# Kernel tuning notes

Measured on AMD Instinct MI355X. Metric: run time of the kernel, lower is better.

## Reference

```python
import jax, jax.numpy as jnp
import numpy as np

D = 512
H = 8
DH = D // H
DFF = 2048
SLOTS = 1024
TOPK = 5
LN_EPS = 1e-5
NORM_EPS = 1e-12


def setup_inputs() -> dict:
    key = jax.random.key(0)
    ks = jax.random.split(key, 12)
    B, S = 8, 1024
    inp = {
        "src": jax.random.normal(ks[0], (B, S, D), dtype=jnp.float32),
        # MultiheadAttention params (torch layout: in_proj [3D, D], out_proj [D, D])
        "in_proj_w": jax.random.normal(ks[1], (3 * D, D), dtype=jnp.float32) * 0.02,
        "in_proj_b": jnp.zeros((3 * D,), dtype=jnp.float32),
        "out_proj_w": jax.random.normal(ks[2], (D, D), dtype=jnp.float32) * 0.02,
        "out_proj_b": jnp.zeros((D,), dtype=jnp.float32),
        # BPBookMemory params
        "memory": jax.random.normal(ks[3], (SLOTS, D), dtype=jnp.float32),
        "retrieval_scale": jnp.asarray(0.1, dtype=jnp.float32),
        # LayerNorms
        "ln1_g": jnp.ones((D,), dtype=jnp.float32),
        "ln1_b": jnp.zeros((D,), dtype=jnp.float32),
        "ln2_g": jnp.ones((D,), dtype=jnp.float32),
        "ln2_b": jnp.zeros((D,), dtype=jnp.float32),
        # FFN (torch Linear layout: [out, in])
        "w1": jax.random.normal(ks[4], (DFF, D), dtype=jnp.float32) * 0.02,
        "b1": jnp.zeros((DFF,), dtype=jnp.float32),
        "w2": jax.random.normal(ks[5], (D, DFF), dtype=jnp.float32) * 0.02,
        "b2": jnp.zeros((D,), dtype=jnp.float32),
    }
    return inp


def _layer_norm(x, g, b):
    mu = jnp.mean(x, axis=-1, keepdims=True)
    var = jnp.var(x, axis=-1, keepdims=True)
    return (x - mu) * jax.lax.rsqrt(var + LN_EPS) * g + b


def _l2_normalize(x):
    n = jnp.linalg.norm(x, axis=-1, keepdims=True)
    return x / jnp.maximum(n, NORM_EPS)


def _forward(src, in_proj_w, in_proj_b, out_proj_w, out_proj_b,
             memory, retrieval_scale, ln1_g, ln1_b, ln2_g, ln2_b,
             w1, b1, w2, b2):
    B, S, _ = src.shape
    # ---- pre-norm self-attention ----
    h = _layer_norm(src, ln1_g, ln1_b)
    qkv = h @ in_proj_w.T + in_proj_b            # [B,S,3D]
    q, k, v = jnp.split(qkv, 3, axis=-1)
    q = q.reshape(B, S, H, DH)
    k = k.reshape(B, S, H, DH)
    v = v.reshape(B, S, H, DH)
    scores = jnp.einsum("bqhd,bkhd->bhqk", q, k) / jnp.sqrt(jnp.float32(DH))
    attn = jax.nn.softmax(scores, axis=-1)
    ctx = jnp.einsum("bhqk,bkhd->bqhd", attn, v).reshape(B, S, D)
    attn_out = ctx @ out_proj_w.T + out_proj_b
    src = src + attn_out
    # ---- BP-Book memory: cosine sim -> topk -> softmax -> gather -> weighted sum ----
    xn = _l2_normalize(src)                      # [B,S,D]
    mn = _l2_normalize(memory)                   # [SLOTS,D]
    sim = xn @ mn.T                              # [B,S,SLOTS]
    topk_scores, topk_idx = jax.lax.top_k(sim, TOPK)
    w = jax.nn.softmax(topk_scores, axis=-1)     # [B,S,TOPK]
    retrieved = memory[topk_idx]                 # [B,S,TOPK,D]
    weighted = jnp.einsum("bskd,bsk->bsd", retrieved, w)
    src = src + retrieval_scale * weighted
    # ---- FFN ----
    h = _layer_norm(src, ln2_g, ln2_b)
    ffn = jax.nn.gelu(h @ w1.T + b1, approximate=False) @ w2.T + b2
    return src + ffn


def reference(src, in_proj_w, in_proj_b, out_proj_w, out_proj_b,
              memory, retrieval_scale, ln1_g, ln1_b, ln2_g, ln2_b,
              w1, b1, w2, b2):
    return _forward(src, in_proj_w, in_proj_b, out_proj_w, out_proj_b,
                    memory, retrieval_scale, ln1_g, ln1_b, ln2_g, ln2_b,
                    w1, b1, w2, b2)
```

## Files before the change

kernel.cpp:

```cpp
#include <hip/hip_runtime.h>
#include <math.h>

#define D_ 512
#define H_ 8
#define DFF_ 2048
#define SLOTS_ 1024
#define TOPK_ 5
#define NCAND_ 8
#define NTOK_ 8192
#define SEQ_ 1024
#define LN_EPS_ 1e-5f

typedef __attribute__((ext_vector_type(8))) short bf16x8;
typedef __attribute__((ext_vector_type(4))) float f32x4;
typedef __attribute__((ext_vector_type(4))) unsigned u32x4;

__device__ inline void split2(float x, unsigned short& hi, unsigned short& lo) {
    unsigned u = __builtin_bit_cast(unsigned, x);
    hi = (unsigned short)(u >> 16);
    float h = __builtin_bit_cast(float, u & 0xFFFF0000u);
    float rem = x - h;
    lo = (unsigned short)(__builtin_bit_cast(unsigned, rem) >> 16);
}

__device__ __forceinline__ void gld16(const void* g, void* l) {
    __builtin_amdgcn_global_load_lds(
        (const __attribute__((address_space(1))) void*)g,
        (__attribute__((address_space(3))) void*)l, 16, 0, 0);
}

__device__ __forceinline__ int SW7(int r) { return (r ^ (r >> 3)) & 7; }
__device__ __forceinline__ const bf16x8* frag(const unsigned short* p, int r, int c) {
    return (const bf16x8*)(p + r * 64 + ((c ^ SW7(r)) << 3));
}

__global__ __launch_bounds__(256) void splitall_kernel(
    const float* __restrict__ inw, const float* __restrict__ outw,
    const float* __restrict__ w1, const float* __restrict__ w2,
    unsigned short* __restrict__ inwh, unsigned short* __restrict__ inwl,
    unsigned short* __restrict__ outwh, unsigned short* __restrict__ outwl,
    unsigned short* __restrict__ w1h, unsigned short* __restrict__ w2h)
{
    const int i = (blockIdx.x * 256 + threadIdx.x) * 4;
    const float* x;
    unsigned short *hh, *ll;
    int base;
    if (i < 786432)       { x = inw;  hh = inwh;  ll = inwl;  base = 0; }
    else if (i < 1048576) { x = outw; hh = outwh; ll = outwl; base = 786432; }
    else if (i < 2097152) { x = w1;   hh = w1h;   ll = nullptr; base = 1048576; }
    else                  { x = w2;   hh = w2h;   ll = nullptr; base = 2097152; }
    const int j = i - base;
    const float4 v = *(const float4*)(x + j);
    const float vv[4] = {v.x, v.y, v.z, v.w};
    unsigned short h[4], l[4];
#pragma unroll
    for (int e = 0; e < 4; ++e) split2(vv[e], h[e], l[e]);
    hh[j + 0] = h[0]; hh[j + 1] = h[1]; hh[j + 2] = h[2]; hh[j + 3] = h[3];
    if (ll) { ll[j + 0] = l[0]; ll[j + 1] = l[1]; ll[j + 2] = l[2]; ll[j + 3] = l[3]; }
}

__global__ __launch_bounds__(256) void ln_kernel(
    const float* __restrict__ x, const float* __restrict__ g,
    const float* __restrict__ be, unsigned short* __restrict__ yh,
    unsigned short* __restrict__ yl)
{
    const int row = blockIdx.x;
    const int t = threadIdx.x;
    const float a = x[(size_t)row * D_ + t];
    const float b = x[(size_t)row * D_ + t + 256];
    float s = a + b;
    float ss = a * a + b * b;
#pragma unroll
    for (int off = 32; off; off >>= 1) {
        s += __shfl_xor(s, off);
        ss += __shfl_xor(ss, off);
    }
    __shared__ float rs[4], rss[4];
    if ((t & 63) == 0) { rs[t >> 6] = s; rss[t >> 6] = ss; }
    __syncthreads();
    s = rs[0] + rs[1] + rs[2] + rs[3];
    ss = rss[0] + rss[1] + rss[2] + rss[3];
    const float mu = s * (1.0f / D_);
    const float var = ss * (1.0f / D_) - mu * mu;
    const float r = rsqrtf(var + LN_EPS_);
    const float y0 = (a - mu) * r * g[t] + be[t];
    const float y1 = (b - mu) * r * g[t + 256] + be[t + 256];
    unsigned short h0, l0, h1, l1;
    split2(y0, h0, l0);
    split2(y1, h1, l1);
    yh[(size_t)row * D_ + t] = h0;
    yh[(size_t)row * D_ + t + 256] = h1;
    yl[(size_t)row * D_ + t] = l0;
    yl[(size_t)row * D_ + t + 256] = l1;
}

__global__ __launch_bounds__(64) void mn_kernel(
    const float* __restrict__ mem, float* __restrict__ mn,
    unsigned short* __restrict__ mnh, unsigned short* __restrict__ mnl)
{
    const int row = blockIdx.x;
    const int lane = threadIdx.x;
    float v[8];
    float ss = 0.0f;
#pragma unroll
    for (int j = 0; j < 8; ++j) {
        v[j] = mem[(size_t)row * D_ + j * 64 + lane];
        ss += v[j] * v[j];
    }
#pragma unroll
    for (int off = 32; off; off >>= 1) ss += __shfl_xor(ss, off);
    const float inv = 1.0f / fmaxf(sqrtf(ss), 1e-12f);
#pragma unroll
    for (int j = 0; j < 8; ++j) {
        const float y = v[j] * inv;
        mn[(size_t)row * D_ + j * 64 + lane] = y;
        unsigned short h, l;
        split2(y, h, l);
        mnh[(size_t)row * D_ + j * 64 + lane] = h;
        mnl[(size_t)row * D_ + j * 64 + lane] = l;
    }
}

enum { EP_QKV = 0, EP_OUTPROJ = 1, EP_SIM = 2, EP_FFN1 = 3, EP_FFN2 = 4 };

template <int SPLIT, int MODE>
__global__ __launch_bounds__(256) void gemm_mf(
    const unsigned short* __restrict__ Ahg, const unsigned short* __restrict__ Alg,
    const unsigned short* __restrict__ Bhg, const unsigned short* __restrict__ Blg,
    const float* __restrict__ bias, const float* __restrict__ res,
    float* __restrict__ C,
    unsigned short* __restrict__ Ch, unsigned short* __restrict__ Cl,
    int M, int N, int K)
{
    __shared__ __align__(16) unsigned short sm[(SPLIT == 3 ? 4 : 2) * 8192];
    unsigned short* Ah = sm;
    unsigned short* Al = sm + 8192;
    unsigned short* Bh = sm + (SPLIT == 3 ? 16384 : 8192);
    unsigned short* Bl = sm + 24576;

    const int tid = threadIdx.x;
    const int lane = tid & 63;
    const int w = tid >> 6;
    const int wr = w >> 1, wc = w & 1;
    const int g = lane >> 4, ln = lane & 15;
    const int m0 = blockIdx.x * 128, n0 = blockIdx.y * 128;
    const int lrow8 = lane >> 3, lchunk = lane & 7;

    const unsigned short* gsrc;
    unsigned short* lds;
    int rbase, rofs, nblk;
    if (SPLIT == 3) {
        nblk = 16; rofs = 0;
        if (w == 0)      { gsrc = Ahg; lds = Ah; rbase = m0; }
        else if (w == 1) { gsrc = Alg; lds = Al; rbase = m0; }
        else if (w == 2) { gsrc = Bhg; lds = Bh; rbase = n0; }
        else             { gsrc = Blg; lds = Bl; rbase = n0; }
    } else {
        nblk = 8; rofs = (w & 1) * 64;
        if (w < 2) { gsrc = Ahg; lds = Ah; rbase = m0; }
        else       { gsrc = Bhg; lds = Bh; rbase = n0; }
    }

    f32x4 acc[4][4];
#pragma unroll
    for (int i = 0; i < 4; ++i)
#pragma unroll
        for (int j = 0; j < 4; ++j) acc[i][j] = (f32x4){0.f, 0.f, 0.f, 0.f};

    for (int k0 = 0; k0 < K; k0 += 64) {
#pragma unroll
        for (int blk = 0; blk < nblk; ++blk) {
            const int row = rofs + blk * 8 + lrow8;
            const int sc = lchunk ^ SW7(row);
            gld16(gsrc + (size_t)(rbase + row) * K + k0 + sc * 8,
                  lds + (rofs + blk * 8) * 64);
        }
        __syncthreads();

#pragma unroll
        for (int ks = 0; ks < 2; ++ks) {
            bf16x8 a_h[4], a_l[4], b_h[4], b_l[4];
#pragma unroll
            for (int mi = 0; mi < 4; ++mi) {
                a_h[mi] = *frag(Ah, wr * 64 + mi * 16 + ln, ks * 4 + g);
                if (SPLIT == 3) a_l[mi] = *frag(Al, wr * 64 + mi * 16 + ln, ks * 4 + g);
            }
#pragma unroll
            for (int ni = 0; ni < 4; ++ni) {
                b_h[ni] = *frag(Bh, wc * 64 + ni * 16 + ln, ks * 4 + g);
                if (SPLIT == 3) b_l[ni] = *frag(Bl, wc * 64 + ni * 16 + ln, ks * 4 + g);
            }
#pragma unroll
            for (int mi = 0; mi < 4; ++mi)
#pragma unroll
                for (int ni = 0; ni < 4; ++ni) {
                    acc[mi][ni] = __builtin_amdgcn_mfma_f32_16x16x32_bf16(
                        a_h[mi], b_h[ni], acc[mi][ni], 0, 0, 0);
                    if (SPLIT == 3) {
                        acc[mi][ni] = __builtin_amdgcn_mfma_f32_16x16x32_bf16(
                            a_h[mi], b_l[ni], acc[mi][ni], 0, 0, 0);
                        acc[mi][ni] = __builtin_amdgcn_mfma_f32_16x16x32_bf16(
                            a_l[mi], b_h[ni], acc[mi][ni], 0, 0, 0);
                    }
                }
        }
        __syncthreads();
    }

#pragma unroll
    for (int mi = 0; mi < 4; ++mi) {
#pragma unroll
        for (int ni = 0; ni < 4; ++ni) {
            const int gn = n0 + wc * 64 + ni * 16 + ln;
            const float bz = (MODE == EP_SIM) ? 0.0f : bias[gn];
#pragma unroll
            for (int r2 = 0; r2 < 4; ++r2) {
                const int gm = m0 + wr * 64 + mi * 16 + g * 4 + r2;
                float v = acc[mi][ni][r2];
                if (MODE == EP_SIM) {
                    C[(size_t)gm * N + gn] = v;
                } else if (MODE == EP_QKV) {
                    v += bz;
                    if (gn < D_) v *= 0.125f;
                    unsigned short h16, l16;
                    split2(v, h16, l16);
                    Ch[(size_t)gm * N + gn] = h16;
                    Cl[(size_t)gm * N + gn] = l16;
                } else if (MODE == EP_OUTPROJ) {
                    v += bz + res[(size_t)gm * N + gn];
                    C[(size_t)gm * N + gn] = v;
                    unsigned short h16, l16;
                    split2(v, h16, l16);
                    Ch[(size_t)gm * N + gn] = h16;
                    Cl[(size_t)gm * N + gn] = l16;
                } else if (MODE == EP_FFN1) {
                    v += bz;
                    v = 0.5f * v * (1.0f + erff(v * 0.70710678118654752f));
                    unsigned short h16, l16;
                    split2(v, h16, l16);
                    Ch[(size_t)gm * N + gn] = h16;
                } else {
                    v += bz + res[(size_t)gm * N + gn];
                    C[(size_t)gm * N + gn] = v;
                }
            }
        }
    }
}

__global__ __launch_bounds__(256, 2) void attn_kernel(
    const unsigned short* __restrict__ qkvh, const unsigned short* __restrict__ qkvl,
    unsigned short* __restrict__ ctxh, unsigned short* __restrict__ ctxl)
{
    const int id = blockIdx.x;
    const int bh = id & 63;
    const int qt = id >> 6;
    const int b = bh >> 3, h = bh & 7;
    const int tok0 = b * SEQ_ + qt * 128;
    const int kbase0 = b * SEQ_;
    const int tid = threadIdx.x;
    const int lane = tid & 63;
    const int w = tid >> 6;
    const int ln = lane & 15, g = lane >> 4;
    const int lrow8 = lane >> 3, lchunk = lane & 7;

    __shared__ __align__(16) unsigned char smb[65536];
    unsigned*       PP  = (unsigned*)smb;
    unsigned short* Qh  = (unsigned short*)smb;
    unsigned short* Ql  = (unsigned short*)(smb + 16384);
    unsigned short* Kh  = (unsigned short*)(smb + 32768);
    unsigned short* Kl  = (unsigned short*)(smb + 40960);
    unsigned short* Vth = (unsigned short*)(smb + 49152);
    unsigned short* Vtl = (unsigned short*)(smb + 57344);

    const int qoff = h * 64, koff = 512 + h * 64, voff = 1024 + h * 64;

#pragma unroll
    for (int blk = 0; blk < 4; ++blk) {
        const int row = w * 32 + blk * 8 + lrow8;
        const int sc = lchunk ^ SW7(row);
        gld16(qkvh + (size_t)(tok0 + row) * 1536 + qoff + sc * 8,
              Qh + (w * 32 + blk * 8) * 64);
        gld16(qkvl + (size_t)(tok0 + row) * 1536 + qoff + sc * 8,
              Ql + (w * 32 + blk * 8) * 64);
    }
    __syncthreads();
    bf16x8 qfh[2][2], qfl[2][2];
#pragma unroll
    for (int qi = 0; qi < 2; ++qi)
#pragma unroll
        for (int ks = 0; ks < 2; ++ks) {
            qfh[qi][ks] = *frag(Qh, w * 32 + qi * 16 + ln, ks * 4 + g);
            qfl[qi][ks] = *frag(Ql, w * 32 + qi * 16 + ln, ks * 4 + g);
        }
    __syncthreads();

    f32x4 o[4][2];
#pragma unroll
    for (int di = 0; di < 4; ++di)
#pragma unroll
        for (int qi = 0; qi < 2; ++qi) o[di][qi] = (f32x4){0.f, 0.f, 0.f, 0.f};
    float mrow2[2] = {-INFINITY, -INFINITY};
    float lrow2[2] = {0.f, 0.f};

    const int p2 = tid & 31, dc = tid >> 5;

    for (int kt = 0; kt < 16; ++kt) {
        const int kb2 = kbase0 + kt * 64;
#pragma unroll
        for (int blk = 0; blk < 2; ++blk) {
            const int row = w * 16 + blk * 8 + lrow8;
            const int sc = lchunk ^ SW7(row);
            gld16(qkvh + (size_t)(kb2 + row) * 1536 + koff + sc * 8,
                  Kh + (w * 16 + blk * 8) * 64);
            gld16(qkvl + (size_t)(kb2 + row) * 1536 + koff + sc * 8,
                  Kl + (w * 16 + blk * 8) * 64);
        }
        {
            const size_t b0 = (size_t)(kb2 + 2 * p2) * 1536 + voff + dc * 8;
            const bf16x8 h0 = *(const bf16x8*)(qkvh + b0);
            const bf16x8 h1 = *(const bf16x8*)(qkvh + b0 + 1536);
            const bf16x8 l0 = *(const bf16x8*)(qkvl + b0);
            const bf16x8 l1 = *(const bf16x8*)(qkvl + b0 + 1536);
#pragma unroll
            for (int j = 0; j < 8; ++j) {
                const int d = dc * 8 + j;
                const int idx = d * 64 + (((p2 >> 2) ^ SW7(d)) << 3) + ((p2 & 3) << 1);
                *(unsigned*)&Vth[idx] = (unsigned)(unsigned short)h0[j]
                                      | ((unsigned)(unsigned short)h1[j] << 16);
                *(unsigned*)&Vtl[idx] = (unsigned)(unsigned short)l0[j]
                                      | ((unsigned)(unsigned short)l1[j] << 16);
            }
        }
        __syncthreads();

        f32x4 s[4][2];
#pragma unroll
        for (int ki = 0; ki < 4; ++ki)
#pragma unroll
            for (int qi = 0; qi < 2; ++qi) s[ki][qi] = (f32x4){0.f, 0.f, 0.f, 0.f};
        __builtin_amdgcn_s_setprio(1);
#pragma unroll
        for (int ks = 0; ks < 2; ++ks) {
            bf16x8 kbh[4], kbl[4];
#pragma unroll
            for (int ki = 0; ki < 4; ++ki) {
                kbh[ki] = *frag(Kh, ki * 16 + ln, ks * 4 + g);
                kbl[ki] = *frag(Kl, ki * 16 + ln, ks * 4 + g);
            }
#pragma unroll
            for (int ki = 0; ki < 4; ++ki)
#pragma unroll
                for (int qi = 0; qi < 2; ++qi) {
                    s[ki][qi] = __builtin_amdgcn_mfma_f32_16x16x32_bf16(kbh[ki], qfh[qi][ks], s[ki][qi], 0, 0, 0);
                    s[ki][qi] = __builtin_amdgcn_mfma_f32_16x16x32_bf16(kbh[ki], qfl[qi][ks], s[ki][qi], 0, 0, 0);
                    s[ki][qi] = __builtin_amdgcn_mfma_f32_16x16x32_bf16(kbl[ki], qfh[qi][ks], s[ki][qi], 0, 0, 0);
                }
        }
        __builtin_amdgcn_s_setprio(0);

        float tm2[2], alpha2[2], psum2[2];
#pragma unroll
        for (int qi = 0; qi < 2; ++qi) {
            float m01 = fmaxf(fmaxf(s[0][qi][0], s[0][qi][1]), fmaxf(s[0][qi][2], s[0][qi][3]));
            float m23 = fmaxf(fmaxf(s[1][qi][0], s[1][qi][1]), fmaxf(s[1][qi][2], s[1][qi][3]));
            float m45 = fmaxf(fmaxf(s[2][qi][0], s[2][qi][1]), fmaxf(s[2][qi][2], s[2][qi][3]));
            float m67 = fmaxf(fmaxf(s[3][qi][0], s[3][qi][1]), fmaxf(s[3][qi][2], s[3][qi][3]));
            tm2[qi] = fmaxf(fmaxf(m01, m23), fmaxf(m45, m67));
        }
#pragma unroll
        for (int qi = 0; qi < 2; ++qi) {
            tm2[qi] = fmaxf(tm2[qi], __shfl_xor(tm2[qi], 16));
            tm2[qi] = fmaxf(tm2[qi], __shfl_xor(tm2[qi], 32));
            const float mnew = fmaxf(mrow2[qi], tm2[qi]);
            alpha2[qi] = __expf(mrow2[qi] - mnew);
            mrow2[qi] = mnew;
            psum2[qi] = 0.f;
        }
#pragma unroll
        for (int qi = 0; qi < 2; ++qi)
#pragma unroll
            for (int ki = 0; ki < 4; ++ki) {
                u32x4 pv;
#pragma unroll
                for (int r2 = 0; r2 < 4; ++r2) {
                    const float p = __expf(s[ki][qi][r2] - mrow2[qi]);
                    psum2[qi] += p;
                    unsigned short h16, l16;
                    split2(p, h16, l16);
                    pv[r2] = (unsigned)h16 | ((unsigned)l16 << 16);
                }
                *(u32x4*)&PP[(w * 32 + qi * 16 + ln) * 64 + ((ki ^ (ln & 3)) << 4) + (g << 2)] = pv;
            }
#pragma unroll
        for (int qi = 0; qi < 2; ++qi) {
            psum2[qi] += __shfl_xor(psum2[qi], 16);
            psum2[qi] += __shfl_xor(psum2[qi], 32);
            lrow2[qi] = lrow2[qi] * alpha2[qi] + psum2[qi];
        }
#pragma unroll
        for (int di = 0; di < 4; ++di)
#pragma unroll
            for (int qi = 0; qi < 2; ++qi)
#pragma unroll
                for (int r2 = 0; r2 < 4; ++r2)
                    o[di][qi][r2] *= alpha2[qi];

        __builtin_amdgcn_s_setprio(1);
#pragma unroll
        for (int ks = 0; ks < 2; ++ks) {
            bf16x8 pah[2], pal[2];
#pragma unroll
            for (int qi = 0; qi < 2; ++qi) {
                const int kiR = 2 * ks + (g >> 1);
                const unsigned* pp = PP + (w * 32 + qi * 16 + ln) * 64
                                     + (((kiR ^ (ln & 3)) << 4) + ((g & 1) << 3));
                const u32x4 q0 = *(const u32x4*)pp;
                const u32x4 q1 = *(const u32x4*)(pp + 4);
                u32x4 hu, lu;
                hu[0] = __builtin_amdgcn_perm(q0[1], q0[0], 0x05040100u);
                hu[1] = __builtin_amdgcn_perm(q0[3], q0[2], 0x05040100u);
                hu[2] = __builtin_amdgcn_perm(q1[1], q1[0], 0x05040100u);
                hu[3] = __builtin_amdgcn_perm(q1[3], q1[2], 0x05040100u);
                lu[0] = __builtin_amdgcn_perm(q0[1], q0[0], 0x07060302u);
                lu[1] = __builtin_amdgcn_perm(q0[3], q0[2], 0x07060302u);
                lu[2] = __builtin_amdgcn_perm(q1[1], q1[0], 0x07060302u);
                lu[3] = __builtin_amdgcn_perm(q1[3], q1[2], 0x07060302u);
                pah[qi] = __builtin_bit_cast(bf16x8, hu);
                pal[qi] = __builtin_bit_cast(bf16x8, lu);
            }
            bf16x8 vbh[4], vbl[4];
#pragma unroll
            for (int di = 0; di < 4; ++di) {
                vbh[di] = *frag(Vth, di * 16 + ln, ks * 4 + g);
                vbl[di] = *frag(Vtl, di * 16 + ln, ks * 4 + g);
            }
#pragma unroll
            for (int di = 0; di < 4; ++di)
#pragma unroll
                for (int qi = 0; qi < 2; ++qi) {
                    o[di][qi] = __builtin_amdgcn_mfma_f32_16x16x32_bf16(vbh[di], pah[qi], o[di][qi], 0, 0, 0);
                    o[di][qi] = __builtin_amdgcn_mfma_f32_16x16x32_bf16(vbh[di], pal[qi], o[di][qi], 0, 0, 0);
                    o[di][qi] = __builtin_amdgcn_mfma_f32_16x16x32_bf16(vbl[di], pah[qi], o[di][qi], 0, 0, 0);
                }
        }
        __builtin_amdgcn_s_setprio(0);
        __syncthreads();
    }

#pragma unroll
    for (int di = 0; di < 4; ++di)
#pragma unroll
        for (int qi = 0; qi < 2; ++qi) {
            const float inv = 1.0f / lrow2[qi];
            u32x4 tv;
#pragma unroll
            for (int r2 = 0; r2 < 4; ++r2) {
                const float v = o[di][qi][r2] * inv;
                unsigned short h16, l16;
                split2(v, h16, l16);
                tv[r2] = (unsigned)h16 | ((unsigned)l16 << 16);
            }
            *(u32x4*)&PP[(w * 32 + qi * 16 + ln) * 64 + ((di ^ (ln & 3)) << 4) + (g << 2)] = tv;
        }
    __syncthreads();
    {
        const int qrow = lane >> 1, halfd = lane & 1;
        const size_t gbase = (size_t)(tok0 + w * 32 + qrow) * D_ + h * 64;
#pragma unroll
        for (int gi = 0; gi < 2; ++gi) {
            const int di = halfd * 2 + gi;
            const unsigned* tp = PP + (w * 32 + qrow) * 64 + ((di ^ (qrow & 3)) << 4);
#pragma unroll
            for (int pr = 0; pr < 2; ++pr) {
                const u32x4 t0 = *(const u32x4*)(tp + pr * 8);
                const u32x4 t1 = *(const u32x4*)(tp + pr * 8 + 4);
                u32x4 hv, lv;
                hv[0] = __builtin_amdgcn_perm(t0[1], t0[0], 0x05040100u);
                hv[1] = __builtin_amdgcn_perm(t0[3], t0[2], 0x05040100u);
                hv[2] = __builtin_amdgcn_perm(t1[1], t1[0], 0x05040100u);
                hv[3] = __builtin_amdgcn_perm(t1[3], t1[2], 0x05040100u);
                lv[0] = __builtin_amdgcn_perm(t0[1], t0[0], 0x07060302u);
                lv[1] = __builtin_amdgcn_perm(t0[3], t0[2], 0x07060302u);
                lv[2] = __builtin_amdgcn_perm(t1[1], t1[0], 0x07060302u);
                lv[3] = __builtin_amdgcn_perm(t1[3], t1[2], 0x07060302u);
                *(u32x4*)(ctxh + gbase + di * 16 + pr * 8) = hv;
                *(u32x4*)(ctxl + gbase + di * 16 + pr * 8) = lv;
            }
        }
    }
}

__global__ __launch_bounds__(64) void topk_kernel(
    const float* __restrict__ sim, const float* __restrict__ src2,
    const float* __restrict__ mn, const float* __restrict__ mem,
    const float* __restrict__ rs_ptr, const float* __restrict__ g2,
    const float* __restrict__ b2, float* __restrict__ out,
    unsigned short* __restrict__ h2h)
{
    const int row = blockIdx.x;
    const int lane = threadIdx.x;
    float v[16];
#pragma unroll
    for (int j = 0; j < 16; ++j)
        v[j] = sim[(size_t)row * SLOTS_ + j * 64 + lane];

    int ci[NCAND_];
#pragma unroll
    for (int t = 0; t < NCAND_; ++t) {
        float bv = -INFINITY;
        int bi = 0x7fffffff;
#pragma unroll
        for (int j = 0; j < 16; ++j) {
            const int idx = j * 64 + lane;
            if (v[j] > bv) { bv = v[j]; bi = idx; }
        }
#pragma unroll
        for (int off = 32; off; off >>= 1) {
            const float ov = __shfl_xor(bv, off);
            const int oi = __shfl_xor(bi, off);
            if (ov > bv || (ov == bv && oi < bi)) { bv = ov; bi = oi; }
        }
        ci[t] = bi;
#pragma unroll
        for (int j = 0; j < 16; ++j)
            if (j * 64 + lane == bi) v[j] = -INFINITY;
    }

    float x[8];
    float ss = 0.0f;
#pragma unroll
    for (int j = 0; j < 8; ++j) {
        x[j] = src2[(size_t)row * D_ + j * 64 + lane];
        ss += x[j] * x[j];
    }
#pragma unroll
    for (int off = 32; off; off >>= 1) ss += __shfl_xor(ss, off);
    const float invn = 1.0f / fmaxf(sqrtf(ss), 1e-12f);

    float rv[NCAND_];
#pragma unroll
    for (int t = 0; t < NCAND_; ++t) {
        const float* mrow = mn + (size_t)ci[t] * D_;
        float acc = 0.0f;
#pragma unroll
        for (int j = 0; j < 8; ++j)
            acc = fmaf(x[j], mrow[j * 64 + lane], acc);
#pragma unroll
        for (int off = 32; off; off >>= 1) acc += __shfl_xor(acc, off);
        rv[t] = acc * invn;
    }

    float wv[TOPK_];
    int wi[TOPK_];
    bool used[NCAND_];
#pragma unroll
    for (int t = 0; t < NCAND_; ++t) used[t] = false;
#pragma unroll
    for (int t = 0; t < TOPK_; ++t) {
        float bv = -INFINITY;
        int bi = 0x7fffffff, bu = 0;
#pragma unroll
        for (int u = 0; u < NCAND_; ++u) {
            if (!used[u] && (rv[u] > bv || (rv[u] == bv && ci[u] < bi))) {
                bv = rv[u]; bi = ci[u]; bu = u;
            }
        }
        used[bu] = true;
        wv[t] = bv;
        wi[t] = bi;
    }

    float m = wv[0];
#pragma unroll
    for (int t = 1; t < TOPK_; ++t) m = fmaxf(m, wv[t]);
    float w[TOPK_], ssum = 0.0f;
#pragma unroll
    for (int t = 0; t < TOPK_; ++t) { w[t] = expf(wv[t] - m); ssum += w[t]; }
    const float scale = rs_ptr[0] / ssum;

    float y[8];
    float s_ = 0.f, ss2 = 0.f;
#pragma unroll
    for (int j = 0; j < 8; ++j) {
        const int d = j * 64 + lane;
        float acc = 0.0f;
#pragma unroll
        for (int t = 0; t < TOPK_; ++t)
            acc += w[t] * mem[(size_t)wi[t] * D_ + d];
        y[j] = x[j] + scale * acc;
        out[(size_t)row * D_ + d] = y[j];
        s_ += y[j];
        ss2 += y[j] * y[j];
    }
#pragma unroll
    for (int off = 32; off; off >>= 1) {
        s_ += __shfl_xor(s_, off);
        ss2 += __shfl_xor(ss2, off);
    }
    const float mu = s_ * (1.0f / D_);
    const float var = ss2 * (1.0f / D_) - mu * mu;
    const float r = rsqrtf(var + LN_EPS_);
#pragma unroll
    for (int j = 0; j < 8; ++j) {
        const int d = j * 64 + lane;
        const float h2 = (y[j] - mu) * r * g2[d] + b2[d];
        unsigned short h16, l16;
        split2(h2, h16, l16);
        h2h[(size_t)row * D_ + d] = h16;
    }
}

extern "C" void kernel_launch(void* const* d_in, const int* in_sizes, int n_in,
                              void* d_out, int out_size, void* d_ws, size_t ws_size,
                              hipStream_t stream)
{
    const float* src  = (const float*)d_in[0];
    const float* inw  = (const float*)d_in[1];
    const float* inb  = (const float*)d_in[2];
    const float* outw = (const float*)d_in[3];
    const float* outb = (const float*)d_in[4];
    const float* mem  = (const float*)d_in[5];
    const float* rs   = (const float*)d_in[6];
    const float* ln1g = (const float*)d_in[7];
    const float* ln1b = (const float*)d_in[8];
    const float* ln2g = (const float*)d_in[9];
    const float* ln2b = (const float*)d_in[10];
    const float* w1   = (const float*)d_in[11];
    const float* b1   = (const float*)d_in[12];
    const float* w2   = (const float*)d_in[13];
    const float* b2   = (const float*)d_in[14];
    float* out = (float*)d_out;
    char* ws = (char*)d_ws;
    const size_t MB = 1024ull * 1024ull;
    typedef unsigned short u16;

    float* mn   = (float*)(ws + 0);
    u16* mnh    = (u16*)(ws + 2 * MB);
    u16* mnl    = (u16*)(ws + 3 * MB);
    u16* h2h    = (u16*)(ws + 4 * MB);
    u16* inwh   = (u16*)(ws + 4 * MB);
    u16* inwl   = (u16*)(ws + 5 * MB + 512 * 1024);
    u16* outwh  = (u16*)(ws + 7 * MB);
    u16* outwl  = (u16*)(ws + 7 * MB + 512 * 1024);
    u16* w1h    = (u16*)(ws + 77 * MB);
    u16* w2h    = (u16*)(ws + 79 * MB);
    u16* hh     = (u16*)(ws + 13 * MB);
    u16* hl     = (u16*)(ws + 21 * MB);
    u16* qkvh   = (u16*)(ws + 29 * MB);
    u16* qkvl   = (u16*)(ws + 53 * MB);
    u16* ctxh   = (u16*)(ws + 13 * MB);
    u16* ctxl   = (u16*)(ws + 21 * MB);
    float* sim  = (float*)(ws + 13 * MB);
    float* src2 = (float*)(ws + 45 * MB);
    u16* src2h  = (u16*)(ws + 61 * MB);
    u16* src2l  = (u16*)(ws + 69 * MB);
    u16* Gbf    = (u16*)(ws + 21 * MB);

    splitall_kernel<<<dim3(3072), dim3(256), 0, stream>>>(
        inw, outw, w1, w2, inwh, inwl, outwh, outwl, w1h, w2h);
    mn_kernel<<<dim3(SLOTS_), dim3(64), 0, stream>>>(mem, mn, mnh, mnl);
    ln_kernel<<<dim3(NTOK_), dim3(256), 0, stream>>>(src, ln1g, ln1b, hh, hl);
    gemm_mf<3, EP_QKV><<<dim3(64, 12), dim3(256), 0, stream>>>(
        hh, hl, inwh, inwl, inb, nullptr, nullptr, qkvh, qkvl, NTOK_, 1536, 512);
    attn_kernel<<<dim3(512), dim3(256), 0, stream>>>(qkvh, qkvl, ctxh, ctxl);
    gemm_mf<3, EP_OUTPROJ><<<dim3(64, 4), dim3(256), 0, stream>>>(
        ctxh, ctxl, outwh, outwl, outb, src, src2, src2h, src2l, NTOK_, 512, 512);
    gemm_mf<3, EP_SIM><<<dim3(64, 8), dim3(256), 0, stream>>>(
        src2h, src2l, mnh, mnl, nullptr, nullptr, sim, nullptr, nullptr, NTOK_, 1024, 512);
    topk_kernel<<<dim3(NTOK_), dim3(64), 0, stream>>>(
        sim, src2, mn, mem, rs, ln2g, ln2b, out, h2h);
    gemm_mf<1, EP_FFN1><<<dim3(64, 16), dim3(256), 0, stream>>>(
        h2h, nullptr, w1h, nullptr, b1, nullptr, nullptr, Gbf, nullptr, NTOK_, 2048, 512);
    gemm_mf<1, EP_FFN2><<<dim3(64, 4), dim3(256), 0, stream>>>(
        Gbf, nullptr, w2h, nullptr, b2, out, out, nullptr, nullptr, NTOK_, 512, 2048);
}
```

Before: 302.9 us.

## Fuse prep kernels, use single-bf16 similarity GEMM, widen attention LDS swizzle

```diff
diff --git a/kernel.cpp b/kernel.cpp
--- a/kernel.cpp
+++ b/kernel.cpp
@@ -14,6 +14,7 @@
 typedef __attribute__((ext_vector_type(8))) short bf16x8;
 typedef __attribute__((ext_vector_type(4))) float f32x4;
 typedef __attribute__((ext_vector_type(4))) unsigned u32x4;
+typedef unsigned short u16;
 
 __device__ inline void split2(float x, unsigned short& hi, unsigned short& lo) {
     unsigned u = __builtin_bit_cast(unsigned, x);
@@ -34,90 +35,86 @@
     return (const bf16x8*)(p + r * 64 + ((c ^ SW7(r)) << 3));
 }
 
-__global__ __launch_bounds__(256) void splitall_kernel(
+__global__ __launch_bounds__(256) void prep_kernel(
     const float* __restrict__ inw, const float* __restrict__ outw,
     const float* __restrict__ w1, const float* __restrict__ w2,
-    unsigned short* __restrict__ inwh, unsigned short* __restrict__ inwl,
-    unsigned short* __restrict__ outwh, unsigned short* __restrict__ outwl,
-    unsigned short* __restrict__ w1h, unsigned short* __restrict__ w2h)
+    const float* __restrict__ mem, const float* __restrict__ src,
+    const float* __restrict__ ln1g, const float* __restrict__ ln1b,
+    u16* __restrict__ inwh, u16* __restrict__ inwl,
+    u16* __restrict__ outwh, u16* __restrict__ outwl,
+    u16* __restrict__ w1h, u16* __restrict__ w2h,
+    float* __restrict__ mn, u16* __restrict__ mnh, u16* __restrict__ mnl,
+    u16* __restrict__ hh, u16* __restrict__ hl)
 {
-    const int i = (blockIdx.x * 256 + threadIdx.x) * 4;
-    const float* x;
-    unsigned short *hh, *ll;
-    int base;
-    if (i < 786432)       { x = inw;  hh = inwh;  ll = inwl;  base = 0; }
-    else if (i < 1048576) { x = outw; hh = outwh; ll = outwl; base = 786432; }
-    else if (i < 2097152) { x = w1;   hh = w1h;   ll = nullptr; base = 1048576; }
-    else                  { x = w2;   hh = w2h;   ll = nullptr; base = 2097152; }
-    const int j = i - base;
-    const float4 v = *(const float4*)(x + j);
-    const float vv[4] = {v.x, v.y, v.z, v.w};
-    unsigned short h[4], l[4];
-#pragma unroll
-    for (int e = 0; e < 4; ++e) split2(vv[e], h[e], l[e]);
-    hh[j + 0] = h[0]; hh[j + 1] = h[1]; hh[j + 2] = h[2]; hh[j + 3] = h[3];
-    if (ll) { ll[j + 0] = l[0]; ll[j + 1] = l[1]; ll[j + 2] = l[2]; ll[j + 3] = l[3]; }
-}
-
-__global__ __launch_bounds__(256) void ln_kernel(
-    const float* __restrict__ x, const float* __restrict__ g,
-    const float* __restrict__ be, unsigned short* __restrict__ yh,
-    unsigned short* __restrict__ yl)
-{
-    const int row = blockIdx.x;
+    const int bid = blockIdx.x;
     const int t = threadIdx.x;
-    const float a = x[(size_t)row * D_ + t];
-    const float b = x[(size_t)row * D_ + t + 256];
-    float s = a + b;
-    float ss = a * a + b * b;
-#pragma unroll
-    for (int off = 32; off; off >>= 1) {
-        s += __shfl_xor(s, off);
-        ss += __shfl_xor(ss, off);
-    }
-    __shared__ float rs[4], rss[4];
-    if ((t & 63) == 0) { rs[t >> 6] = s; rss[t >> 6] = ss; }
-    __syncthreads();
-    s = rs[0] + rs[1] + rs[2] + rs[3];
-    ss = rss[0] + rss[1] + rss[2] + rss[3];
-    const float mu = s * (1.0f / D_);
-    const float var = ss * (1.0f / D_) - mu * mu;
-    const float r = rsqrtf(var + LN_EPS_);
-    const float y0 = (a - mu) * r * g[t] + be[t];
-    const float y1 = (b - mu) * r * g[t + 256] + be[t + 256];
-    unsigned short h0, l0, h1, l1;
-    split2(y0, h0, l0);
-    split2(y1, h1, l1);
-    yh[(size_t)row * D_ + t] = h0;
-    yh[(size_t)row * D_ + t + 256] = h1;
-    yl[(size_t)row * D_ + t] = l0;
-    yl[(size_t)row * D_ + t + 256] = l1;
-}
-
-__global__ __launch_bounds__(64) void mn_kernel(
-    const float* __restrict__ mem, float* __restrict__ mn,
-    unsigned short* __restrict__ mnh, unsigned short* __restrict__ mnl)
-{
-    const int row = blockIdx.x;
-    const int lane = threadIdx.x;
-    float v[8];
-    float ss = 0.0f;
-#pragma unroll
-    for (int j = 0; j < 8; ++j) {
-        v[j] = mem[(size_t)row * D_ + j * 64 + lane];
-        ss += v[j] * v[j];
-    }
-#pragma unroll
-    for (int off = 32; off; off >>= 1) ss += __shfl_xor(ss, off);
-    const float inv = 1.0f / fmaxf(sqrtf(ss), 1e-12f);
-#pragma unroll
-    for (int j = 0; j < 8; ++j) {
-        const float y = v[j] * inv;
-        mn[(size_t)row * D_ + j * 64 + lane] = y;
-        unsigned short h, l;
-        split2(y, h, l);
-        mnh[(size_t)row * D_ + j * 64 + lane] = h;
-        mnl[(size_t)row * D_ + j * 64 + lane] = l;
+    if (bid < 3072) {
+        const int i = (bid * 256 + t) * 4;
+        const float* x;
+        u16 *hhp, *llp;
+        int base;
+        if (i < 786432)       { x = inw;  hhp = inwh;  llp = inwl;  base = 0; }
+        else if (i < 1048576) { x = outw; hhp = outwh; llp = outwl; base = 786432; }
+        else if (i < 2097152) { x = w1;   hhp = w1h;   llp = nullptr; base = 1048576; }
+        else                  { x = w2;   hhp = w2h;   llp = nullptr; base = 2097152; }
+        const int j = i - base;
+        const float4 v = *(const float4*)(x + j);
+        const float vv[4] = {v.x, v.y, v.z, v.w};
+        u16 h[4], l[4];
+#pragma unroll
+        for (int e = 0; e < 4; ++e) split2(vv[e], h[e], l[e]);
+        hhp[j + 0] = h[0]; hhp[j + 1] = h[1]; hhp[j + 2] = h[2]; hhp[j + 3] = h[3];
+        if (llp) { llp[j + 0] = l[0]; llp[j + 1] = l[1]; llp[j + 2] = l[2]; llp[j + 3] = l[3]; }
+    } else if (bid < 3328) {
+        const int row = (bid - 3072) * 4 + (t >> 6);
+        const int lane = t & 63;
+        float v[8];
+        float ss = 0.0f;
+#pragma unroll
+        for (int j = 0; j < 8; ++j) {
+            v[j] = mem[(size_t)row * D_ + j * 64 + lane];
+            ss += v[j] * v[j];
+        }
+#pragma unroll
+        for (int off = 32; off; off >>= 1) ss += __shfl_xor(ss, off);
+        const float inv = 1.0f / fmaxf(sqrtf(ss), 1e-12f);
+#pragma unroll
+        for (int j = 0; j < 8; ++j) {
+            const float y = v[j] * inv;
+            mn[(size_t)row * D_ + j * 64 + lane] = y;
+            u16 h, l;
+            split2(y, h, l);
+            mnh[(size_t)row * D_ + j * 64 + lane] = h;
+            mnl[(size_t)row * D_ + j * 64 + lane] = l;
+        }
+    } else {
+        const int row = bid - 3328;
+        const float a = src[(size_t)row * D_ + t];
+        const float b = src[(size_t)row * D_ + t + 256];
+        float s = a + b;
+        float ss = a * a + b * b;
+#pragma unroll
+        for (int off = 32; off; off >>= 1) {
+            s += __shfl_xor(s, off);
+            ss += __shfl_xor(ss, off);
+        }
+        __shared__ float rs[4], rss[4];
+        if ((t & 63) == 0) { rs[t >> 6] = s; rss[t >> 6] = ss; }
+        __syncthreads();
+        s = rs[0] + rs[1] + rs[2] + rs[3];
+        ss = rss[0] + rss[1] + rss[2] + rss[3];
+        const float mu = s * (1.0f / D_);
+        const float var = ss * (1.0f / D_) - mu * mu;
+        const float r = rsqrtf(var + LN_EPS_);
+        const float y0 = (a - mu) * r * ln1g[t] + ln1b[t];
+        const float y1 = (b - mu) * r * ln1g[t + 256] + ln1b[t + 256];
+        u16 h0, l0, h1, l1;
+        split2(y0, h0, l0);
+        split2(y1, h1, l1);
+        hh[(size_t)row * D_ + t] = h0;
+        hh[(size_t)row * D_ + t + 256] = h1;
+        hl[(size_t)row * D_ + t] = l0;
+        hl[(size_t)row * D_ + t + 256] = l1;
     }
 }
 
@@ -232,7 +229,6 @@
                     unsigned short h16, l16;
                     split2(v, h16, l16);
                     Ch[(size_t)gm * N + gn] = h16;
-                    Cl[(size_t)gm * N + gn] = l16;
                 } else if (MODE == EP_FFN1) {
                     v += bz;
                     v = 0.5f * v * (1.0f + erff(v * 0.70710678118654752f));
@@ -390,7 +386,7 @@
                     split2(p, h16, l16);
                     pv[r2] = (unsigned)h16 | ((unsigned)l16 << 16);
                 }
-                *(u32x4*)&PP[(w * 32 + qi * 16 + ln) * 64 + ((ki ^ (ln & 3)) << 4) + (g << 2)] = pv;
+                *(u32x4*)&PP[(w * 32 + qi * 16 + ln) * 64 + (((ki * 4 + g) ^ (ln & 7)) << 2)] = pv;
             }
 #pragma unroll
         for (int qi = 0; qi < 2; ++qi) {
@@ -412,11 +408,10 @@
             bf16x8 pah[2], pal[2];
 #pragma unroll
             for (int qi = 0; qi < 2; ++qi) {
-                const int kiR = 2 * ks + (g >> 1);
-                const unsigned* pp = PP + (w * 32 + qi * 16 + ln) * 64
-                                     + (((kiR ^ (ln & 3)) << 4) + ((g & 1) << 3));
-                const u32x4 q0 = *(const u32x4*)pp;
-                const u32x4 q1 = *(const u32x4*)(pp + 4);
+                const unsigned* rowp = PP + (w * 32 + qi * 16 + ln) * 64;
+                const int c0 = (2 * ks + (g >> 1)) * 4 + (g & 1) * 2;
+                const u32x4 q0 = *(const u32x4*)(rowp + (((c0    ) ^ (ln & 7)) << 2));
+                const u32x4 q1 = *(const u32x4*)(rowp + (((c0 + 1) ^ (ln & 7)) << 2));
                 u32x4 hu, lu;
                 hu[0] = __builtin_amdgcn_perm(q0[1], q0[0], 0x05040100u);
                 hu[1] = __builtin_amdgcn_perm(q0[3], q0[2], 0x05040100u);
@@ -461,20 +456,21 @@
                 split2(v, h16, l16);
                 tv[r2] = (unsigned)h16 | ((unsigned)l16 << 16);
             }
-            *(u32x4*)&PP[(w * 32 + qi * 16 + ln) * 64 + ((di ^ (ln & 3)) << 4) + (g << 2)] = tv;
+            *(u32x4*)&PP[(w * 32 + qi * 16 + ln) * 64 + (((di * 4 + g) ^ (ln & 7)) << 2)] = tv;
         }
     __syncthreads();
     {
         const int qrow = lane >> 1, halfd = lane & 1;
+        const unsigned* rowp = PP + (w * 32 + qrow) * 64;
         const size_t gbase = (size_t)(tok0 + w * 32 + qrow) * D_ + h * 64;
 #pragma unroll
         for (int gi = 0; gi < 2; ++gi) {
             const int di = halfd * 2 + gi;
-            const unsigned* tp = PP + (w * 32 + qrow) * 64 + ((di ^ (qrow & 3)) << 4);
 #pragma unroll
             for (int pr = 0; pr < 2; ++pr) {
-                const u32x4 t0 = *(const u32x4*)(tp + pr * 8);
-                const u32x4 t1 = *(const u32x4*)(tp + pr * 8 + 4);
+                const int c = di * 4 + pr * 2;
+                const u32x4 t0 = *(const u32x4*)(rowp + (((c    ) ^ (qrow & 7)) << 2));
+                const u32x4 t1 = *(const u32x4*)(rowp + (((c + 1) ^ (qrow & 7)) << 2));
                 u32x4 hv, lv;
                 hv[0] = __builtin_amdgcn_perm(t0[1], t0[0], 0x05040100u);
                 hv[1] = __builtin_amdgcn_perm(t0[3], t0[2], 0x05040100u);
@@ -576,7 +572,7 @@
     for (int t = 1; t < TOPK_; ++t) m = fmaxf(m, wv[t]);
     float w[TOPK_], ssum = 0.0f;
 #pragma unroll
-    for (int t = 0; t < TOPK_; ++t) { w[t] = expf(wv[t] - m); ssum += w[t]; }
+    for (int t = 0; t < TOPK_; ++t) { w[t] = __expf(wv[t] - m); ssum += w[t]; }
     const float scale = rs_ptr[0] / ssum;
 
     float y[8];
@@ -633,7 +629,6 @@
     float* out = (float*)d_out;
     char* ws = (char*)d_ws;
     const size_t MB = 1024ull * 1024ull;
-    typedef unsigned short u16;
 
     float* mn   = (float*)(ws + 0);
     u16* mnh    = (u16*)(ws + 2 * MB);
@@ -654,20 +649,18 @@
     float* sim  = (float*)(ws + 13 * MB);
     float* src2 = (float*)(ws + 45 * MB);
     u16* src2h  = (u16*)(ws + 61 * MB);
-    u16* src2l  = (u16*)(ws + 69 * MB);
     u16* Gbf    = (u16*)(ws + 21 * MB);
 
-    splitall_kernel<<<dim3(3072), dim3(256), 0, stream>>>(
-        inw, outw, w1, w2, inwh, inwl, outwh, outwl, w1h, w2h);
-    mn_kernel<<<dim3(SLOTS_), dim3(64), 0, stream>>>(mem, mn, mnh, mnl);
-    ln_kernel<<<dim3(NTOK_), dim3(256), 0, stream>>>(src, ln1g, ln1b, hh, hl);
+    prep_kernel<<<dim3(11520), dim3(256), 0, stream>>>(
+        inw, outw, w1, w2, mem, src, ln1g, ln1b,
+        inwh, inwl, outwh, outwl, w1h, w2h, mn, mnh, mnl, hh, hl);
     gemm_mf<3, EP_QKV><<<dim3(64, 12), dim3(256), 0, stream>>>(
         hh, hl, inwh, inwl, inb, nullptr, nullptr, qkvh, qkvl, NTOK_, 1536, 512);
     attn_kernel<<<dim3(512), dim3(256), 0, stream>>>(qkvh, qkvl, ctxh, ctxl);
     gemm_mf<3, EP_OUTPROJ><<<dim3(64, 4), dim3(256), 0, stream>>>(
-        ctxh, ctxl, outwh, outwl, outb, src, src2, src2h, src2l, NTOK_, 512, 512);
-    gemm_mf<3, EP_SIM><<<dim3(64, 8), dim3(256), 0, stream>>>(
-        src2h, src2l, mnh, mnl, nullptr, nullptr, sim, nullptr, nullptr, NTOK_, 1024, 512);
+        ctxh, ctxl, outwh, outwl, outb, src, src2, src2h, nullptr, NTOK_, 512, 512);
+    gemm_mf<1, EP_SIM><<<dim3(64, 8), dim3(256), 0, stream>>>(
+        src2h, nullptr, mnh, nullptr, nullptr, nullptr, sim, nullptr, nullptr, NTOK_, 1024, 512);
     topk_kernel<<<dim3(NTOK_), dim3(64), 0, stream>>>(
         sim, src2, mn, mem, rs, ln2g, ln2b, out, h2h);
     gemm_mf<1, EP_FFN1><<<dim3(64, 16), dim3(256), 0, stream>>>(
```

After: 282.9 us. -6.6%, faster.
